# Kernel tuning notes

Measured on AMD Instinct MI355X. Metric: run time of the kernel, lower is better.

The kernel has to match this reference:

```python
import jax, jax.numpy as jnp
import numpy as np

N, Wd = 1000000, 20
EPS = 1e-16


def setup_inputs() -> dict:
    key = jax.random.key(0)
    ks = jax.random.split(key, 40)
    def rn(i, shape, scale=0.05):
        return jax.random.normal(ks[i], shape, dtype=jnp.float32) * scale
    inp = {
        "X": rn(0, (1, 14), 1.0),
        "read_weights": jax.nn.sigmoid(rn(1, (1, N), 1.0)),
        "write_weights": jax.nn.sigmoid(rn(2, (1, N), 1.0)),
        "Memory": jnp.full((N, Wd), 1e-6, dtype=jnp.float32),
        "read_head": jax.nn.sigmoid(rn(3, (1, Wd), 1.0)),
        "W1": rn(4, (48, 14)), "b1": rn(5, (48,)),
        "W2": rn(6, (72, 48)), "b2": rn(7, (72,)),
        "Wxi": rn(8, ((Wd + 6) * 2 + 2 * Wd, 72)), "bxi": rn(9, ((Wd + 6) * 2 + 2 * Wd,)),
        "Wz": rn(10, (3, 72)), "bz": rn(11, (3,)),
        "Wv": rn(12, (20, 325)), "bv": rn(13, (20,)),
        "aW1": rn(14, (110, 40)), "ab1": rn(15, (110,)),
        "aW2": rn(16, (190, 110)), "ab2": rn(17, (190,)),
        "aW3": rn(18, (270, 190)), "ab3": rn(19, (270,)),
        "aW4": rn(20, (325, 270)), "ab4": rn(21, (325,)),
        "mW1": rn(22, (110, 40)), "mb1": rn(23, (110,)),
        "mW2": rn(24, (190, 110)), "mb2": rn(25, (190,)),
        "mW3": rn(26, (270, 190)), "mb3": rn(27, (270,)),
        "mW4": rn(28, (325, 270)), "mb4": rn(29, (325,)),
    }
    return inp


def _alu(x, W1, b1, W2, b2, W3, b3, W4, b4):
    x = jax.nn.relu(x @ W1.T + b1)
    x = jax.nn.relu(x @ W2.T + b2)
    x = jax.nn.relu(x @ W3.T + b3)
    return jax.nn.softmax(x @ W4.T + b4, axis=-1)


def _head_params(p):  # p: (1, Wd+6)
    k = jnp.tanh(p[0, :Wd])[None, :]              # (1, Wd)
    g = jax.nn.sigmoid(p[0, Wd])
    s = jax.nn.softmax(p[0, Wd + 1:Wd + 4])        # (3,)
    gamma = 1.0 + jax.nn.softplus(p[0, Wd + 4])
    beta = jax.nn.softplus(p[0, Wd + 5])
    return k, g, s, gamma, beta


def _address(Memory, k, beta, g, s, gamma, w_prev):
    Me = Memory + EPS                              # (N, Wd)
    ke = k + EPS                                   # (1, Wd)
    num = (Me @ ke.T)[:, 0]                        # (N,)
    den = jnp.maximum(jnp.linalg.norm(Me, axis=-1), 1e-8) * \
          jnp.maximum(jnp.linalg.norm(ke, axis=-1), 1e-8)
    w_c = jax.nn.softmax((num / den) * beta)       # (N,)
    w_g = g * w_c + (1.0 - g) * w_prev             # (1, N)
    pad = jnp.concatenate([w_g[:, -1:], w_g, w_g[:, :1]], axis=1)  # (1, N+2)
    w_r = s[0] * pad[:, :N] + s[1] * pad[:, 1:N + 1] + s[2] * pad[:, 2:]
    w = w_r ** gamma
    return w / (jnp.sum(w, axis=1, keepdims=True) + EPS)


def reference(X, read_weights, write_weights, Memory, read_head,
              W1, b1, W2, b2, Wxi, bxi, Wz, bz, Wv, bv,
              aW1, ab1, aW2, ab2, aW3, ab3, aW4, ab4,
              mW1, mb1, mW2, mb2, mW3, mb3, mW4, mb4):
    h = X @ W1.T + b1                # (1, 48)  (no activation, faithful)
    h = h @ W2.T + b2                # (1, 72)
    xi = h @ Wxi.T + bxi             # (1, 92)
    zeta = h @ Wz.T + bz             # (1, 3)

    rp = xi[0, :Wd + 6][None, :]
    wp = xi[0, Wd + 6:(Wd + 6) * 2][None, :]
    erase = jax.nn.sigmoid(xi[0, (Wd + 6) * 2:(Wd + 6) * 2 + Wd][None, :])
    add = jnp.tanh(xi[0, (Wd + 6) * 2 + Wd:(Wd + 6) * 2 + 2 * Wd][None, :])

    k, g, s, gamma, beta = _head_params(rp)
    rw = _address(Memory, k, beta, g, s, gamma, read_weights)
    k, g, s, gamma, beta = _head_params(wp)
    ww = _address(Memory, k, beta, g, s, gamma, write_weights)

    new_read_head = rw @ Memory                    # (1, Wd)
    alu_in = jnp.concatenate([read_head, new_read_head], axis=1)  # (1, 2*Wd)

    rho = jax.nn.sigmoid(zeta[0, 0])
    alu_head = jax.nn.softmax(zeta[:, 1:], axis=-1)  # (1, 2)
    out_add = _alu(alu_in, aW1, ab1, aW2, ab2, aW3, ab3, aW4, ab4)
    out_mul = _alu(alu_in, mW1, mb1, mW2, mb2, mW3, mb3, mW4, mb4)
    out = alu_head[0, 0] * out_add + alu_head[0, 1] * out_mul  # (1, 325)

    v = out @ Wv.T + bv                              # (1, 20)
    add = rho * add + (1.0 - rho) * v

    new_memory = Memory * (1.0 - ww.T @ erase) + ww.T @ add  # (N, Wd)
    return out, rw, ww, new_memory, new_read_head
```

## Files before the change

kernel.cpp:

```cpp
#include <hip/hip_runtime.h>
#include <math.h>

#define NN 1000000
#define WD 20
#define NB 977
#define PST 1024

#define OUT_OFF 0
#define RW_OFF  325
#define WW_OFF  1000325
#define NM_OFF  2000325
#define NRH_OFF 22000325

__device__ __forceinline__ float sigmoidf_(float x){ return 1.0f/(1.0f+expf(-x)); }
__device__ __forceinline__ float softplusf_(float x){ return (x>30.f)?x:log1pf(expf(x)); }

__global__ void k_head(const float* __restrict__ X,
                       const float* __restrict__ W1, const float* __restrict__ b1,
                       const float* __restrict__ W2, const float* __restrict__ b2,
                       const float* __restrict__ Wxi, const float* __restrict__ bxi,
                       const float* __restrict__ Wz, const float* __restrict__ bz,
                       float* __restrict__ P){
  __shared__ float h1[48], h2[72], xi[92], zeta[3];
  int t = threadIdx.x;
  if(t<48){ float a=b1[t]; const float* w=W1+t*14; for(int c=0;c<14;c++) a+=X[c]*w[c]; h1[t]=a; }
  __syncthreads();
  if(t<72){ float a=b2[t]; const float* w=W2+t*48; for(int c=0;c<48;c++) a+=h1[c]*w[c]; h2[t]=a; }
  __syncthreads();
  if(t<92){ float a=bxi[t]; const float* w=Wxi+t*72; for(int c=0;c<72;c++) a+=h2[c]*w[c]; xi[t]=a; }
  else if(t<95){ int z=t-92; float a=bz[z]; const float* w=Wz+z*72; for(int c=0;c<72;c++) a+=h2[c]*w[c]; zeta[z]=a; }
  __syncthreads();
  if(t<20){
    P[0+t]  = tanhf(xi[t]);
    P[32+t] = tanhf(xi[26+t]);
    P[64+t] = sigmoidf_(xi[52+t]);
    P[84+t] = tanhf(xi[72+t]);
  }
  if(t==32){
    const float* p = xi;
    float g=sigmoidf_(p[20]);
    float a0=p[21],a1=p[22],a2=p[23];
    float mx=fmaxf(a0,fmaxf(a1,a2));
    float e0=expf(a0-mx),e1=expf(a1-mx),e2=expf(a2-mx),es=e0+e1+e2;
    float gamma=1.0f+softplusf_(p[24]);
    float beta=softplusf_(p[25]);
    float n2=0.f; for(int j=0;j<20;j++){ float ke=tanhf(p[j])+1e-16f; n2+=ke*ke; }
    P[20]=g; P[21]=e0/es; P[22]=e1/es; P[23]=e2/es; P[24]=gamma; P[25]=beta;
    P[26]=fmaxf(sqrtf(n2),1e-8f);
  }
  if(t==33){
    const float* p = xi+26;
    float g=sigmoidf_(p[20]);
    float a0=p[21],a1=p[22],a2=p[23];
    float mx=fmaxf(a0,fmaxf(a1,a2));
    float e0=expf(a0-mx),e1=expf(a1-mx),e2=expf(a2-mx),es=e0+e1+e2;
    float gamma=1.0f+softplusf_(p[24]);
    float beta=softplusf_(p[25]);
    float n2=0.f; for(int j=0;j<20;j++){ float ke=tanhf(p[j])+1e-16f; n2+=ke*ke; }
    P[52]=g; P[53]=e0/es; P[54]=e1/es; P[55]=e2/es; P[56]=gamma; P[57]=beta;
    P[58]=fmaxf(sqrtf(n2),1e-8f);
  }
  if(t==34){
    P[104]=sigmoidf_(zeta[0]);
    float mx=fmaxf(zeta[1],zeta[2]);
    float e1=expf(zeta[1]-mx), e2=expf(zeta[2]-mx);
    P[105]=e1/(e1+e2); P[106]=e2/(e1+e2);
  }
}

__global__ __launch_bounds__(256) void k_scores(const float* __restrict__ M, const float* __restrict__ P,
                         float* __restrict__ score_r, float* __restrict__ score_w,
                         float4* __restrict__ pms){
  int t=threadIdx.x, b=blockIdx.x;
  float kr[20], kw[20];
#pragma unroll
  for(int j=0;j<20;j++){ kr[j]=P[j]+1e-16f; kw[j]=P[32+j]+1e-16f; }
  float betar=P[25], betaw=P[57], knr=P[26], knw=P[58];
  float sR[4], sW[4];
#pragma unroll
  for(int p=0;p<4;p++){
    int i=b*1024+p*256+t;
    if(i<NN){
      const float4* row=(const float4*)(M+(size_t)i*WD);
      float dr=0.f,dw=0.f,n2=0.f;
#pragma unroll
      for(int q=0;q<5;q++){
        float4 v=row[q];
        float m0=v.x+1e-16f,m1=v.y+1e-16f,m2=v.z+1e-16f,m3=v.w+1e-16f;
        dr+=m0*kr[4*q]+m1*kr[4*q+1]+m2*kr[4*q+2]+m3*kr[4*q+3];
        dw+=m0*kw[4*q]+m1*kw[4*q+1]+m2*kw[4*q+2]+m3*kw[4*q+3];
        n2+=m0*m0+m1*m1+m2*m2+m3*m3;
      }
      float nm=fmaxf(sqrtf(n2),1e-8f);
      sR[p]=betar*(dr/(nm*knr));
      sW[p]=betaw*(dw/(nm*knw));
      score_r[i]=sR[p]; score_w[i]=sW[p];
    } else { sR[p]=-3.0e38f; sW[p]=-3.0e38f; }
  }
  __shared__ float r1[256], r2[256];
  __shared__ double d1[256], d2[256];
  float lm1=fmaxf(fmaxf(sR[0],sR[1]),fmaxf(sR[2],sR[3]));
  float lm2=fmaxf(fmaxf(sW[0],sW[1]),fmaxf(sW[2],sW[3]));
  r1[t]=lm1; r2[t]=lm2; __syncthreads();
  for(int o=128;o>0;o>>=1){ if(t<o){ r1[t]=fmaxf(r1[t],r1[t+o]); r2[t]=fmaxf(r2[t],r2[t+o]); } __syncthreads(); }
  float mb1=r1[0], mb2=r2[0]; __syncthreads();
  double s1=0.0,s2=0.0;
#pragma unroll
  for(int p=0;p<4;p++){ s1+=(double)expf(sR[p]-mb1); s2+=(double)expf(sW[p]-mb2); }
  d1[t]=s1; d2[t]=s2; __syncthreads();
  for(int o=128;o>0;o>>=1){ if(t<o){ d1[t]+=d1[t+o]; d2[t]+=d2[t+o]; } __syncthreads(); }
  if(t==0) pms[b]=make_float4(mb1,mb2,(float)d1[0],(float)d2[0]);
}

__global__ __launch_bounds__(256) void k_shift(const float* __restrict__ score_r, const float* __restrict__ score_w,
                        const float* __restrict__ wpr, const float* __restrict__ wpw,
                        const float* __restrict__ M, const float* __restrict__ P,
                        const float4* __restrict__ pms,
                        float* __restrict__ w_r_out, float* __restrict__ w_w_out,
                        double* __restrict__ pZ, double* __restrict__ pnrhT){
  __shared__ float r1[256], r2[256];
  __shared__ double d1[256], d2[256];
  __shared__ float bmS[4];
  __shared__ float wsum[4][20];
  int t=threadIdx.x, b=blockIdx.x;
  float4 v[4];
#pragma unroll
  for(int k=0;k<4;k++){
    int idx=t+k*256;
    v[k] = (idx<NB) ? pms[idx] : make_float4(-3.0e38f,-3.0e38f,0.f,0.f);
  }
  float lm1=fmaxf(fmaxf(v[0].x,v[1].x),fmaxf(v[2].x,v[3].x));
  float lm2=fmaxf(fmaxf(v[0].y,v[1].y),fmaxf(v[2].y,v[3].y));
  r1[t]=lm1; r2[t]=lm2; __syncthreads();
  for(int o=128;o>0;o>>=1){ if(t<o){ r1[t]=fmaxf(r1[t],r1[t+o]); r2[t]=fmaxf(r2[t],r2[t+o]); } __syncthreads(); }
  if(t==0){ bmS[0]=r1[0]; bmS[1]=r2[0]; } __syncthreads();
  float mr=bmS[0], mw=bmS[1];
  double s1=0.0,s2=0.0;
#pragma unroll
  for(int k=0;k<4;k++){
    s1 += (double)v[k].z * (double)expf(v[k].x-mr);
    s2 += (double)v[k].w * (double)expf(v[k].y-mw);
  }
  d1[t]=s1; d2[t]=s2; __syncthreads();
  for(int o=128;o>0;o>>=1){ if(t<o){ d1[t]+=d1[t+o]; d2[t]+=d2[t+o]; } __syncthreads(); }
  if(t==0){ bmS[2]=(float)d1[0]; bmS[3]=(float)d2[0]; } __syncthreads();
  float Sr=bmS[2], Sw=bmS[3];
  float gr=P[20], s0r=P[21], s1r=P[22], s2r=P[23], gar=P[24];
  float gw=P[52], s0w=P[53], s1w=P[54], s2w=P[55], gaw=P[56];
  float omgr=1.0f-gr, omgw=1.0f-gw;
  float acc[20];
#pragma unroll
  for(int j=0;j<20;j++) acc[j]=0.f;
  double zr=0.0, zw=0.0;
  for(int p=0;p<4;p++){
    int i=b*1024+p*256+t;
    if(i<NN){
      int im1=(i==0)?(NN-1):(i-1);
      int ip1=(i==NN-1)?0:(i+1);
      float wgrm = gr*(expf(score_r[im1]-mr)/Sr) + omgr*wpr[im1];
      float wgr0 = gr*(expf(score_r[i  ]-mr)/Sr) + omgr*wpr[i  ];
      float wgrp = gr*(expf(score_r[ip1]-mr)/Sr) + omgr*wpr[ip1];
      float wgwm = gw*(expf(score_w[im1]-mw)/Sw) + omgw*wpw[im1];
      float wgw0 = gw*(expf(score_w[i  ]-mw)/Sw) + omgw*wpw[i  ];
      float wgwp = gw*(expf(score_w[ip1]-mw)/Sw) + omgw*wpw[ip1];
      float wr = powf(s0r*wgrm + s1r*wgr0 + s2r*wgrp, gar);
      float ww = powf(s0w*wgwm + s1w*wgw0 + s2w*wgwp, gaw);
      w_r_out[i]=wr; w_w_out[i]=ww;
      zr+=(double)wr; zw+=(double)ww;
      const float4* row=(const float4*)(M+(size_t)i*WD);
#pragma unroll
      for(int q=0;q<5;q++){
        float4 mv=row[q];
        acc[4*q+0]+=wr*mv.x; acc[4*q+1]+=wr*mv.y; acc[4*q+2]+=wr*mv.z; acc[4*q+3]+=wr*mv.w;
      }
    }
  }
  d1[t]=zr; d2[t]=zw; __syncthreads();
  for(int o=128;o>0;o>>=1){ if(t<o){ d1[t]+=d1[t+o]; d2[t]+=d2[t+o]; } __syncthreads(); }
  if(t==0){ pZ[2*b]=d1[0]; pZ[2*b+1]=d2[0]; }
#pragma unroll
  for(int j=0;j<20;j++){
    for(int off=32;off>0;off>>=1) acc[j]+=__shfl_down(acc[j],off,64);
  }
  int wave=t>>6, lane=t&63;
  if(lane==0){
#pragma unroll
    for(int j=0;j<20;j++) wsum[wave][j]=acc[j];
  }
  __syncthreads();
  if(t<20){
    double s=(double)wsum[0][t]+(double)wsum[1][t]+(double)wsum[2][t]+(double)wsum[3][t];
    pnrhT[(size_t)t*PST+b]=s;
  }
}

__global__ __launch_bounds__(256) void k_nrh(const double* __restrict__ pZ, const double* __restrict__ pnrhT,
                      const float* __restrict__ read_head,
                      float* __restrict__ in40, float* __restrict__ out, double* __restrict__ Sd){
  __shared__ double dd[256];
  __shared__ double bZ[2];
  int t=threadIdx.x, j=blockIdx.x;
  double a=0.0,c=0.0;
  for(int idx=t; idx<NB; idx+=256){ a+=pZ[2*idx]; c+=pZ[2*idx+1]; }
  dd[t]=a; __syncthreads();
  for(int o=128;o>0;o>>=1){ if(t<o) dd[t]+=dd[t+o]; __syncthreads(); }
  if(t==0) bZ[0]=dd[0]; __syncthreads();
  dd[t]=c; __syncthreads();
  for(int o=128;o>0;o>>=1){ if(t<o) dd[t]+=dd[t+o]; __syncthreads(); }
  if(t==0) bZ[1]=dd[0]; __syncthreads();
  if(j==0 && t==0){ Sd[0]=bZ[0]; Sd[1]=bZ[1]; }
  double s=0.0;
  for(int idx=t; idx<NB; idx+=256) s+=pnrhT[(size_t)j*PST+idx];
  dd[t]=s; __syncthreads();
  for(int o=128;o>0;o>>=1){ if(t<o) dd[t]+=dd[t+o]; __syncthreads(); }
  if(t==0){
    float nv=(float)(dd[0]/(bZ[0]+1e-16));
    in40[20+j]=nv; out[NRH_OFF+j]=nv;
    in40[j]=read_head[j];
  }
}

__global__ __launch_bounds__(256) void k_layer(const float* __restrict__ Wa, const float* __restrict__ ba,
                        const float* __restrict__ Wm, const float* __restrict__ bm,
                        const float* __restrict__ inA, const float* __restrict__ inM,
                        float* __restrict__ oA, float* __restrict__ oM,
                        int rows, int K, int RB, int doRelu){
  int net = (blockIdx.x >= RB) ? 1 : 0;
  const float* W = net ? Wm : Wa;
  const float* bb = net ? bm : ba;
  const float* in = net ? inM : inA;
  float* o = net ? oM : oA;
  int wave=threadIdx.x>>6, lane=threadIdx.x&63;
  int r=(blockIdx.x - net*RB)*4 + wave;
  if(r>=rows) return;
  const float* w = W + (size_t)r*K;
  float a=0.f;
  for(int c=lane; c<K; c+=64) a += w[c]*in[c];
  for(int off=32;off>0;off>>=1) a += __shfl_down(a,off,64);
  if(lane==0){
    float vv=a+bb[r];
    o[r]= doRelu ? fmaxf(vv,0.f) : vv;
  }
}

__global__ __launch_bounds__(512) void k_fin(const float* __restrict__ h4a, const float* __restrict__ h4m,
                      const float* __restrict__ Wv, const float* __restrict__ bv,
                      float* __restrict__ P, float* __restrict__ out){
  __shared__ float red[512];
  __shared__ float A[325], B[325];
  __shared__ float sc[2];
  int t=threadIdx.x;
  float la=(t<325)?h4a[t]:-3.0e38f;
  red[t]=la; __syncthreads();
  for(int o=256;o>0;o>>=1){ if(t<o) red[t]=fmaxf(red[t],red[t+o]); __syncthreads(); }
  if(t==0) sc[0]=red[0]; __syncthreads();
  float ea=(t<325)?expf(la-sc[0]):0.f;
  red[t]=ea; __syncthreads();
  for(int o=256;o>0;o>>=1){ if(t<o) red[t]+=red[t+o]; __syncthreads(); }
  if(t==0) sc[1]=red[0]; __syncthreads();
  if(t<325) A[t]=ea/sc[1];
  __syncthreads();
  float lm=(t<325)?h4m[t]:-3.0e38f;
  red[t]=lm; __syncthreads();
  for(int o=256;o>0;o>>=1){ if(t<o) red[t]=fmaxf(red[t],red[t+o]); __syncthreads(); }
  if(t==0) sc[0]=red[0]; __syncthreads();
  float em=(t<325)?expf(lm-sc[0]):0.f;
  red[t]=em; __syncthreads();
  for(int o=256;o>0;o>>=1){ if(t<o) red[t]+=red[t+o]; __syncthreads(); }
  if(t==0) sc[1]=red[0]; __syncthreads();
  if(t<325) B[t]=em/sc[1];
  __syncthreads();
  float ah0=P[105], ah1=P[106];
  if(t<325){ float ov=ah0*A[t]+ah1*B[t]; out[OUT_OFF+t]=ov; A[t]=ov; }
  __syncthreads();
  int wave=t>>6, lane=t&63;
  for(int r=wave; r<20; r+=8){
    const float* w=Wv+(size_t)r*325;
    float a=0.f;
    for(int c=lane;c<325;c+=64) a+=w[c]*A[c];
    for(int off=32;off>0;off>>=1) a+=__shfl_down(a,off,64);
    if(lane==0){
      float vv=a+bv[r];
      float rho=P[104];
      P[112+r]=rho*P[84+r]+(1.0f-rho)*vv;
    }
  }
}

__global__ __launch_bounds__(256) void k_memupd(const float* __restrict__ M,
                         float* __restrict__ w_r, float* __restrict__ w_w,
                         const float* __restrict__ P, const double* __restrict__ Sd,
                         float* __restrict__ nm){
  int t=threadIdx.x, b=blockIdx.x;
  float er[20], af[20];
#pragma unroll
  for(int j=0;j<20;j++){ er[j]=P[64+j]; af[j]=P[112+j]; }
  float Zr=(float)Sd[0]+1e-16f, Zw=(float)Sd[1]+1e-16f;
  for(int p=0;p<4;p++){
    int i=b*1024+p*256+t;
    if(i<NN){
      float wrn=w_r[i]/Zr;
      float wwn=w_w[i]/Zw;
      w_r[i]=wrn; w_w[i]=wwn;
      const float4* row=(const float4*)(M+(size_t)i*WD);
      float4* dst=(float4*)(nm+(size_t)i*WD);
#pragma unroll
      for(int q=0;q<5;q++){
        float4 v=row[q];
        float4 o;
        o.x=v.x*(1.0f-wwn*er[4*q+0])+wwn*af[4*q+0];
        o.y=v.y*(1.0f-wwn*er[4*q+1])+wwn*af[4*q+1];
        o.z=v.z*(1.0f-wwn*er[4*q+2])+wwn*af[4*q+2];
        o.w=v.w*(1.0f-wwn*er[4*q+3])+wwn*af[4*q+3];
        dst[q]=o;
      }
    }
  }
}

extern "C" void kernel_launch(void* const* d_in, const int* in_sizes, int n_in,
                              void* d_out, int out_size, void* d_ws, size_t ws_size,
                              hipStream_t stream) {
  const float* X    =(const float*)d_in[0];
  const float* rwp  =(const float*)d_in[1];
  const float* wwp  =(const float*)d_in[2];
  const float* Mem  =(const float*)d_in[3];
  const float* rhd  =(const float*)d_in[4];
  const float* W1   =(const float*)d_in[5];
  const float* b1   =(const float*)d_in[6];
  const float* W2   =(const float*)d_in[7];
  const float* b2   =(const float*)d_in[8];
  const float* Wxi  =(const float*)d_in[9];
  const float* bxi  =(const float*)d_in[10];
  const float* Wz   =(const float*)d_in[11];
  const float* bz   =(const float*)d_in[12];
  const float* Wv   =(const float*)d_in[13];
  const float* bv   =(const float*)d_in[14];
  const float* aW1  =(const float*)d_in[15];
  const float* ab1  =(const float*)d_in[16];
  const float* aW2  =(const float*)d_in[17];
  const float* ab2  =(const float*)d_in[18];
  const float* aW3  =(const float*)d_in[19];
  const float* ab3  =(const float*)d_in[20];
  const float* aW4  =(const float*)d_in[21];
  const float* ab4  =(const float*)d_in[22];
  const float* mW1  =(const float*)d_in[23];
  const float* mb1  =(const float*)d_in[24];
  const float* mW2  =(const float*)d_in[25];
  const float* mb2  =(const float*)d_in[26];
  const float* mW3  =(const float*)d_in[27];
  const float* mb3  =(const float*)d_in[28];
  const float* mW4  =(const float*)d_in[29];
  const float* mb4  =(const float*)d_in[30];

  float* out = (float*)d_out;
  char* ws = (char*)d_ws;
  float*  P     = (float*) (ws + 0);
  float4* pms   = (float4*)(ws + 4096);
  double* pZ    = (double*)(ws + 32768);
  double* pnrhT = (double*)(ws + 65536);
  double* Sd    = (double*)(ws + 229376);
  float*  in40  = (float*) (ws + 229504);
  float*  F     = (float*) (ws + 229760);
  float *h1a=F,      *h1m=F+110;
  float *h2a=F+220,  *h2m=F+410;
  float *h3a=F+600,  *h3m=F+870;
  float *h4a=F+1140, *h4m=F+1465;

  float* score_r = out + NM_OFF;
  float* score_w = score_r + NN;
  float* w_r = out + RW_OFF;
  float* w_w = out + WW_OFF;
  float* nm  = out + NM_OFF;

  k_head<<<1,128,0,stream>>>(X,W1,b1,W2,b2,Wxi,bxi,Wz,bz,P);
  k_scores<<<NB,256,0,stream>>>(Mem,P,score_r,score_w,pms);
  k_shift<<<NB,256,0,stream>>>(score_r,score_w,rwp,wwp,Mem,P,pms,w_r,w_w,pZ,pnrhT);
  k_nrh<<<20,256,0,stream>>>(pZ,pnrhT,rhd,in40,out,Sd);
  k_layer<<<56,256,0,stream>>>(aW1,ab1,mW1,mb1,in40,in40,h1a,h1m,110,40,28,1);
  k_layer<<<96,256,0,stream>>>(aW2,ab2,mW2,mb2,h1a,h1m,h2a,h2m,190,110,48,1);
  k_layer<<<136,256,0,stream>>>(aW3,ab3,mW3,mb3,h2a,h2m,h3a,h3m,270,190,68,1);
  k_layer<<<164,256,0,stream>>>(aW4,ab4,mW4,mb4,h3a,h3m,h4a,h4m,325,270,82,0);
  k_fin<<<1,512,0,stream>>>(h4a,h4m,Wv,bv,P,out);
  k_memupd<<<NB,256,0,stream>>>(Mem,w_r,w_w,P,Sd,nm);
}
```

Measured before the change: 120.5 us.

## Fuse head MLP into scores kernel and stage Memory rows through LDS

Each scores block now recomputes the small controller MLP redundantly instead of running a separate single-block kernel, which removes one launch and its serial dependency. Memory rows (20 floats, 80 bytes each) are loaded with coalesced float4 accesses into a shared-memory tile in the scores, shift and memory-update kernels, and the update kernel also writes back through LDS. The read and write scores are interleaved into one float2 array. The cost is extra barriers, about 20KB of LDS per block, and redundant MLP work in all 977 blocks.

```diff
diff --git a/kernel.cpp b/kernel.cpp
--- a/kernel.cpp
+++ b/kernel.cpp
@@ -2,6 +2,7 @@
 #include <math.h>
 
 #define NN 1000000
+#define NF4 5000000
 #define WD 20
 #define NB 977
 #define PST 1024
@@ -15,26 +16,29 @@
 __device__ __forceinline__ float sigmoidf_(float x){ return 1.0f/(1.0f+expf(-x)); }
 __device__ __forceinline__ float softplusf_(float x){ return (x>30.f)?x:log1pf(expf(x)); }
 
-__global__ void k_head(const float* __restrict__ X,
-                       const float* __restrict__ W1, const float* __restrict__ b1,
-                       const float* __restrict__ W2, const float* __restrict__ b2,
-                       const float* __restrict__ Wxi, const float* __restrict__ bxi,
-                       const float* __restrict__ Wz, const float* __restrict__ bz,
-                       float* __restrict__ P){
-  __shared__ float h1[48], h2[72], xi[92], zeta[3];
-  int t = threadIdx.x;
+__global__ __launch_bounds__(256) void k_scores(
+    const float* __restrict__ X,
+    const float* __restrict__ W1, const float* __restrict__ b1,
+    const float* __restrict__ W2, const float* __restrict__ b2,
+    const float* __restrict__ Wxi, const float* __restrict__ bxi,
+    const float* __restrict__ Wz, const float* __restrict__ bz,
+    const float* __restrict__ M, float* __restrict__ Pg,
+    float2* __restrict__ sc2, float4* __restrict__ pms){
+  __shared__ float4 ld[1280];
+  __shared__ float h1[48], h2[72], xi[95], sP[132];
+  int t=threadIdx.x, b=blockIdx.x;
   if(t<48){ float a=b1[t]; const float* w=W1+t*14; for(int c=0;c<14;c++) a+=X[c]*w[c]; h1[t]=a; }
   __syncthreads();
   if(t<72){ float a=b2[t]; const float* w=W2+t*48; for(int c=0;c<48;c++) a+=h1[c]*w[c]; h2[t]=a; }
   __syncthreads();
   if(t<92){ float a=bxi[t]; const float* w=Wxi+t*72; for(int c=0;c<72;c++) a+=h2[c]*w[c]; xi[t]=a; }
-  else if(t<95){ int z=t-92; float a=bz[z]; const float* w=Wz+z*72; for(int c=0;c<72;c++) a+=h2[c]*w[c]; zeta[z]=a; }
+  else if(t<95){ int z=t-92; float a=bz[z]; const float* w=Wz+z*72; for(int c=0;c<72;c++) a+=h2[c]*w[c]; xi[92+z]=a; }
   __syncthreads();
   if(t<20){
-    P[0+t]  = tanhf(xi[t]);
-    P[32+t] = tanhf(xi[26+t]);
-    P[64+t] = sigmoidf_(xi[52+t]);
-    P[84+t] = tanhf(xi[72+t]);
+    sP[0+t]  = tanhf(xi[t]);
+    sP[32+t] = tanhf(xi[26+t]);
+    sP[64+t] = sigmoidf_(xi[52+t]);
+    sP[84+t] = tanhf(xi[72+t]);
   }
   if(t==32){
     const float* p = xi;
@@ -45,8 +49,8 @@
     float gamma=1.0f+softplusf_(p[24]);
     float beta=softplusf_(p[25]);
     float n2=0.f; for(int j=0;j<20;j++){ float ke=tanhf(p[j])+1e-16f; n2+=ke*ke; }
-    P[20]=g; P[21]=e0/es; P[22]=e1/es; P[23]=e2/es; P[24]=gamma; P[25]=beta;
-    P[26]=fmaxf(sqrtf(n2),1e-8f);
+    sP[20]=g; sP[21]=e0/es; sP[22]=e1/es; sP[23]=e2/es; sP[24]=gamma; sP[25]=beta;
+    sP[26]=fmaxf(sqrtf(n2),1e-8f);
   }
   if(t==33){
     const float* p = xi+26;
@@ -57,48 +61,54 @@
     float gamma=1.0f+softplusf_(p[24]);
     float beta=softplusf_(p[25]);
     float n2=0.f; for(int j=0;j<20;j++){ float ke=tanhf(p[j])+1e-16f; n2+=ke*ke; }
-    P[52]=g; P[53]=e0/es; P[54]=e1/es; P[55]=e2/es; P[56]=gamma; P[57]=beta;
-    P[58]=fmaxf(sqrtf(n2),1e-8f);
+    sP[52]=g; sP[53]=e0/es; sP[54]=e1/es; sP[55]=e2/es; sP[56]=gamma; sP[57]=beta;
+    sP[58]=fmaxf(sqrtf(n2),1e-8f);
   }
   if(t==34){
-    P[104]=sigmoidf_(zeta[0]);
-    float mx=fmaxf(zeta[1],zeta[2]);
-    float e1=expf(zeta[1]-mx), e2=expf(zeta[2]-mx);
-    P[105]=e1/(e1+e2); P[106]=e2/(e1+e2);
-  }
-}
-
-__global__ __launch_bounds__(256) void k_scores(const float* __restrict__ M, const float* __restrict__ P,
-                         float* __restrict__ score_r, float* __restrict__ score_w,
-                         float4* __restrict__ pms){
-  int t=threadIdx.x, b=blockIdx.x;
+    sP[104]=sigmoidf_(xi[92]);
+    float mx=fmaxf(xi[93],xi[94]);
+    float e1=expf(xi[93]-mx), e2=expf(xi[94]-mx);
+    sP[105]=e1/(e1+e2); sP[106]=e2/(e1+e2);
+  }
+  __syncthreads();
+  if(b==0 && t<132) Pg[t]=sP[t];
   float kr[20], kw[20];
 #pragma unroll
-  for(int j=0;j<20;j++){ kr[j]=P[j]+1e-16f; kw[j]=P[32+j]+1e-16f; }
-  float betar=P[25], betaw=P[57], knr=P[26], knw=P[58];
+  for(int j=0;j<20;j++){ kr[j]=sP[j]+1e-16f; kw[j]=sP[32+j]+1e-16f; }
+  float betar=sP[25], betaw=sP[57], knr=sP[26], knw=sP[58];
+  const float4* Mf4=(const float4*)M;
   float sR[4], sW[4];
-#pragma unroll
   for(int p=0;p<4;p++){
-    int i=b*1024+p*256+t;
+    int rb=b*1024+p*256;
+    size_t f4b=(size_t)rb*5;
+#pragma unroll
+    for(int k=0;k<5;k++){
+      size_t idx=f4b+(size_t)(k*256+t);
+      ld[k*256+t] = (idx<NF4)?Mf4[idx]:make_float4(0.f,0.f,0.f,0.f);
+    }
+    __syncthreads();
+    int i=rb+t;
+    float srv=-3.0e38f, swv=-3.0e38f;
     if(i<NN){
-      const float4* row=(const float4*)(M+(size_t)i*WD);
       float dr=0.f,dw=0.f,n2=0.f;
 #pragma unroll
       for(int q=0;q<5;q++){
-        float4 v=row[q];
+        float4 v=ld[t*5+q];
         float m0=v.x+1e-16f,m1=v.y+1e-16f,m2=v.z+1e-16f,m3=v.w+1e-16f;
         dr+=m0*kr[4*q]+m1*kr[4*q+1]+m2*kr[4*q+2]+m3*kr[4*q+3];
         dw+=m0*kw[4*q]+m1*kw[4*q+1]+m2*kw[4*q+2]+m3*kw[4*q+3];
         n2+=m0*m0+m1*m1+m2*m2+m3*m3;
       }
       float nm=fmaxf(sqrtf(n2),1e-8f);
-      sR[p]=betar*(dr/(nm*knr));
-      sW[p]=betaw*(dw/(nm*knw));
-      score_r[i]=sR[p]; score_w[i]=sW[p];
-    } else { sR[p]=-3.0e38f; sW[p]=-3.0e38f; }
-  }
-  __shared__ float r1[256], r2[256];
-  __shared__ double d1[256], d2[256];
+      srv=betar*(dr/(nm*knr));
+      swv=betaw*(dw/(nm*knw));
+      sc2[i]=make_float2(srv,swv);
+    }
+    sR[p]=srv; sW[p]=swv;
+    __syncthreads();
+  }
+  float* r1=(float*)ld; float* r2=r1+256;
+  double* d1=(double*)(r1+512); double* d2=d1+256;
   float lm1=fmaxf(fmaxf(sR[0],sR[1]),fmaxf(sR[2],sR[3]));
   float lm2=fmaxf(fmaxf(sW[0],sW[1]),fmaxf(sW[2],sW[3]));
   r1[t]=lm1; r2[t]=lm2; __syncthreads();
@@ -112,25 +122,26 @@
   if(t==0) pms[b]=make_float4(mb1,mb2,(float)d1[0],(float)d2[0]);
 }
 
-__global__ __launch_bounds__(256) void k_shift(const float* __restrict__ score_r, const float* __restrict__ score_w,
+__global__ __launch_bounds__(256) void k_shift(const float2* __restrict__ sc2,
                         const float* __restrict__ wpr, const float* __restrict__ wpw,
                         const float* __restrict__ M, const float* __restrict__ P,
                         const float4* __restrict__ pms,
                         float* __restrict__ w_r_out, float* __restrict__ w_w_out,
                         double* __restrict__ pZ, double* __restrict__ pnrhT){
-  __shared__ float r1[256], r2[256];
-  __shared__ double d1[256], d2[256];
+  __shared__ float4 ld[1280];
   __shared__ float bmS[4];
-  __shared__ float wsum[4][20];
+  float* r1=(float*)ld; float* r2=r1+256;
+  double* d1=(double*)(r1+512); double* d2=d1+256;
+  float* wsum=(float*)(d2+256);
   int t=threadIdx.x, b=blockIdx.x;
-  float4 v[4];
+  float4 v4[4];
 #pragma unroll
   for(int k=0;k<4;k++){
     int idx=t+k*256;
-    v[k] = (idx<NB) ? pms[idx] : make_float4(-3.0e38f,-3.0e38f,0.f,0.f);
-  }
-  float lm1=fmaxf(fmaxf(v[0].x,v[1].x),fmaxf(v[2].x,v[3].x));
-  float lm2=fmaxf(fmaxf(v[0].y,v[1].y),fmaxf(v[2].y,v[3].y));
+    v4[k] = (idx<NB) ? pms[idx] : make_float4(-3.0e38f,-3.0e38f,0.f,0.f);
+  }
+  float lm1=fmaxf(fmaxf(v4[0].x,v4[1].x),fmaxf(v4[2].x,v4[3].x));
+  float lm2=fmaxf(fmaxf(v4[0].y,v4[1].y),fmaxf(v4[2].y,v4[3].y));
   r1[t]=lm1; r2[t]=lm2; __syncthreads();
   for(int o=128;o>0;o>>=1){ if(t<o){ r1[t]=fmaxf(r1[t],r1[t+o]); r2[t]=fmaxf(r2[t],r2[t+o]); } __syncthreads(); }
   if(t==0){ bmS[0]=r1[0]; bmS[1]=r2[0]; } __syncthreads();
@@ -138,8 +149,8 @@
   double s1=0.0,s2=0.0;
 #pragma unroll
   for(int k=0;k<4;k++){
-    s1 += (double)v[k].z * (double)expf(v[k].x-mr);
-    s2 += (double)v[k].w * (double)expf(v[k].y-mw);
+    s1 += (double)v4[k].z * (double)expf(v4[k].x-mr);
+    s2 += (double)v4[k].w * (double)expf(v4[k].y-mw);
   }
   d1[t]=s1; d2[t]=s2; __syncthreads();
   for(int o=128;o>0;o>>=1){ if(t<o){ d1[t]+=d1[t+o]; d2[t]+=d2[t+o]; } __syncthreads(); }
@@ -148,36 +159,47 @@
   float gr=P[20], s0r=P[21], s1r=P[22], s2r=P[23], gar=P[24];
   float gw=P[52], s0w=P[53], s1w=P[54], s2w=P[55], gaw=P[56];
   float omgr=1.0f-gr, omgw=1.0f-gw;
+  const float4* Mf4=(const float4*)M;
   float acc[20];
 #pragma unroll
   for(int j=0;j<20;j++) acc[j]=0.f;
   double zr=0.0, zw=0.0;
   for(int p=0;p<4;p++){
-    int i=b*1024+p*256+t;
+    int rb=b*1024+p*256;
+    size_t f4b=(size_t)rb*5;
+#pragma unroll
+    for(int k=0;k<5;k++){
+      size_t idx=f4b+(size_t)(k*256+t);
+      ld[k*256+t] = (idx<NF4)?Mf4[idx]:make_float4(0.f,0.f,0.f,0.f);
+    }
+    __syncthreads();
+    int i=rb+t;
     if(i<NN){
       int im1=(i==0)?(NN-1):(i-1);
       int ip1=(i==NN-1)?0:(i+1);
-      float wgrm = gr*(expf(score_r[im1]-mr)/Sr) + omgr*wpr[im1];
-      float wgr0 = gr*(expf(score_r[i  ]-mr)/Sr) + omgr*wpr[i  ];
-      float wgrp = gr*(expf(score_r[ip1]-mr)/Sr) + omgr*wpr[ip1];
-      float wgwm = gw*(expf(score_w[im1]-mw)/Sw) + omgw*wpw[im1];
-      float wgw0 = gw*(expf(score_w[i  ]-mw)/Sw) + omgw*wpw[i  ];
-      float wgwp = gw*(expf(score_w[ip1]-mw)/Sw) + omgw*wpw[ip1];
+      float2 scm=sc2[im1], sc0=sc2[i], scp=sc2[ip1];
+      float wgrm = gr*(expf(scm.x-mr)/Sr) + omgr*wpr[im1];
+      float wgr0 = gr*(expf(sc0.x-mr)/Sr) + omgr*wpr[i  ];
+      float wgrp = gr*(expf(scp.x-mr)/Sr) + omgr*wpr[ip1];
+      float wgwm = gw*(expf(scm.y-mw)/Sw) + omgw*wpw[im1];
+      float wgw0 = gw*(expf(sc0.y-mw)/Sw) + omgw*wpw[i  ];
+      float wgwp = gw*(expf(scp.y-mw)/Sw) + omgw*wpw[ip1];
       float wr = powf(s0r*wgrm + s1r*wgr0 + s2r*wgrp, gar);
       float ww = powf(s0w*wgwm + s1w*wgw0 + s2w*wgwp, gaw);
       w_r_out[i]=wr; w_w_out[i]=ww;
       zr+=(double)wr; zw+=(double)ww;
-      const float4* row=(const float4*)(M+(size_t)i*WD);
 #pragma unroll
       for(int q=0;q<5;q++){
-        float4 mv=row[q];
+        float4 mv=ld[t*5+q];
         acc[4*q+0]+=wr*mv.x; acc[4*q+1]+=wr*mv.y; acc[4*q+2]+=wr*mv.z; acc[4*q+3]+=wr*mv.w;
       }
     }
+    __syncthreads();
   }
   d1[t]=zr; d2[t]=zw; __syncthreads();
   for(int o=128;o>0;o>>=1){ if(t<o){ d1[t]+=d1[t+o]; d2[t]+=d2[t+o]; } __syncthreads(); }
   if(t==0){ pZ[2*b]=d1[0]; pZ[2*b+1]=d2[0]; }
+  __syncthreads();
 #pragma unroll
   for(int j=0;j<20;j++){
     for(int off=32;off>0;off>>=1) acc[j]+=__shfl_down(acc[j],off,64);
@@ -185,11 +207,11 @@
   int wave=t>>6, lane=t&63;
   if(lane==0){
 #pragma unroll
-    for(int j=0;j<20;j++) wsum[wave][j]=acc[j];
+    for(int j=0;j<20;j++) wsum[wave*20+j]=acc[j];
   }
   __syncthreads();
   if(t<20){
-    double s=(double)wsum[0][t]+(double)wsum[1][t]+(double)wsum[2][t]+(double)wsum[3][t];
+    double s=(double)wsum[0*20+t]+(double)wsum[1*20+t]+(double)wsum[2*20+t]+(double)wsum[3*20+t];
     pnrhT[(size_t)t*PST+b]=s;
   }
 }
@@ -291,30 +313,46 @@
                          float* __restrict__ w_r, float* __restrict__ w_w,
                          const float* __restrict__ P, const double* __restrict__ Sd,
                          float* __restrict__ nm){
+  __shared__ float4 ld[1280];
   int t=threadIdx.x, b=blockIdx.x;
   float er[20], af[20];
 #pragma unroll
   for(int j=0;j<20;j++){ er[j]=P[64+j]; af[j]=P[112+j]; }
   float Zr=(float)Sd[0]+1e-16f, Zw=(float)Sd[1]+1e-16f;
+  const float4* Mf4=(const float4*)M;
+  float4* nmf4=(float4*)nm;
   for(int p=0;p<4;p++){
-    int i=b*1024+p*256+t;
+    int rb=b*1024+p*256;
+    size_t f4b=(size_t)rb*5;
+#pragma unroll
+    for(int k=0;k<5;k++){
+      size_t idx=f4b+(size_t)(k*256+t);
+      if(idx<NF4) ld[k*256+t]=Mf4[idx];
+    }
+    __syncthreads();
+    int i=rb+t;
     if(i<NN){
       float wrn=w_r[i]/Zr;
       float wwn=w_w[i]/Zw;
       w_r[i]=wrn; w_w[i]=wwn;
-      const float4* row=(const float4*)(M+(size_t)i*WD);
-      float4* dst=(float4*)(nm+(size_t)i*WD);
 #pragma unroll
       for(int q=0;q<5;q++){
-        float4 v=row[q];
+        float4 v=ld[t*5+q];
         float4 o;
         o.x=v.x*(1.0f-wwn*er[4*q+0])+wwn*af[4*q+0];
         o.y=v.y*(1.0f-wwn*er[4*q+1])+wwn*af[4*q+1];
         o.z=v.z*(1.0f-wwn*er[4*q+2])+wwn*af[4*q+2];
         o.w=v.w*(1.0f-wwn*er[4*q+3])+wwn*af[4*q+3];
-        dst[q]=o;
+        ld[t*5+q]=o;
       }
     }
+    __syncthreads();
+#pragma unroll
+    for(int k=0;k<5;k++){
+      size_t idx=f4b+(size_t)(k*256+t);
+      if(idx<NF4) nmf4[idx]=ld[k*256+t];
+    }
+    __syncthreads();
   }
 }
 
@@ -355,27 +393,25 @@
 
   float* out = (float*)d_out;
   char* ws = (char*)d_ws;
-  float*  P     = (float*) (ws + 0);
-  float4* pms   = (float4*)(ws + 4096);
-  double* pZ    = (double*)(ws + 32768);
-  double* pnrhT = (double*)(ws + 65536);
-  double* Sd    = (double*)(ws + 229376);
-  float*  in40  = (float*) (ws + 229504);
-  float*  F     = (float*) (ws + 229760);
+  float*    P     = (float*)   (ws + 0);
+  double*   Sd    = (double*)  (ws + 2048);
+  float*    in40  = (float*)   (ws + 2304);
+  float*    F     = (float*)   (ws + 4096);
+  float4*   pms   = (float4*)  (ws + 16384);
+  double*   pZ    = (double*)  (ws + 32768);
+  double*   pnrhT = (double*)  (ws + 65536);
   float *h1a=F,      *h1m=F+110;
   float *h2a=F+220,  *h2m=F+410;
   float *h3a=F+600,  *h3m=F+870;
   float *h4a=F+1140, *h4m=F+1465;
 
-  float* score_r = out + NM_OFF;
-  float* score_w = score_r + NN;
-  float* w_r = out + RW_OFF;
-  float* w_w = out + WW_OFF;
-  float* nm  = out + NM_OFF;
-
-  k_head<<<1,128,0,stream>>>(X,W1,b1,W2,b2,Wxi,bxi,Wz,bz,P);
-  k_scores<<<NB,256,0,stream>>>(Mem,P,score_r,score_w,pms);
-  k_shift<<<NB,256,0,stream>>>(score_r,score_w,rwp,wwp,Mem,P,pms,w_r,w_w,pZ,pnrhT);
+  float2* sc2 = (float2*)(out + NM_OFF);
+  float*  w_r = out + RW_OFF;
+  float*  w_w = out + WW_OFF;
+  float*  nm  = out + NM_OFF;
+
+  k_scores<<<NB,256,0,stream>>>(X,W1,b1,W2,b2,Wxi,bxi,Wz,bz,Mem,P,sc2,pms);
+  k_shift<<<NB,256,0,stream>>>(sc2,rwp,wwp,Mem,P,pms,w_r,w_w,pZ,pnrhT);
   k_nrh<<<20,256,0,stream>>>(pZ,pnrhT,rhd,in40,out,Sd);
   k_layer<<<56,256,0,stream>>>(aW1,ab1,mW1,mb1,in40,in40,h1a,h1m,110,40,28,1);
   k_layer<<<96,256,0,stream>>>(aW2,ab2,mW2,mb2,h1a,h1m,h2a,h2m,190,110,48,1);
```

Result: faster. 116.5 us (-3.3%).
